# Performance work log

Measured on AMD Instinct MI355X. Metric: run time of the kernel, lower is better.

## Reference

```python
import jax, jax.numpy as jnp
import numpy as np

N_HEAD = 8


def _norm(x):
    # torch: (x - x.mean()) / x.std()  -- global, unbiased std (ddof=1)
    return (x - x.mean()) / x.std(ddof=1)


def _floyd_block2(x, w_qkv, scale):
    # x: [b, n, n, c]; w_qkv: [5c, c] (torch Linear weight layout)
    x = _norm(x)
    b, n, _, c = x.shape
    qkv = x @ w_qkv.T  # [b, n, n, 5c]
    q, k1, k2, v1, v2 = jnp.split(qkv, 5, axis=-1)

    def heads(t):  # 'b i j (h d) -> b h i j d'
        return t.reshape(b, n, n, N_HEAD, c // N_HEAD).transpose(0, 3, 1, 2, 4)

    q, k1, k2, v1, v2 = map(heads, (q, k1, k2, v1, v2))
    # pivotal attention: for pair (i,j) attend over pivot p with two k/v branches
    s = (jnp.einsum('bhijd,bhipd->bhijp', q, k1)
         + jnp.einsum('bhijd,bhpjd->bhijp', q, k2)) * scale  # [b,h,i,j,p]
    a = jax.nn.softmax(s, axis=-1)
    o = (jnp.einsum('bhijp,bhipd->bhijd', a, v1)
         + jnp.einsum('bhijp,bhpjd->bhijd', a, v2))
    # 'b h i j d -> b i j (h d)'
    return o.transpose(0, 2, 3, 1, 4).reshape(b, n, n, c)


def setup_inputs() -> dict:
    key = jax.random.key(0)
    k1, k2, k3, k4 = jax.random.split(key, 4)
    b, n, c, depth = 4, 96, 256, 4
    adj = jax.random.randint(k1, (b, n, n), 0, 2, dtype=jnp.int64)
    emb_w = jax.random.normal(k2, (128, c), dtype=jnp.float32)  # std 1.0 per init_weights
    qkv_w = jax.random.normal(k3, (depth, 5 * c, c), dtype=jnp.float32) * (c ** -0.5)
    head_w = jax.random.normal(k4, (c, c), dtype=jnp.float32) * 0.02
    head_b = jnp.zeros((c,), dtype=jnp.float32)
    return {'adj': adj, 'emb_w': emb_w, 'qkv_w': qkv_w,
            'head_w': head_w, 'head_b': head_b}


def reference(adj, emb_w, qkv_w, head_w, head_b):
    c = emb_w.shape[1]
    head_dim = c // N_HEAD
    scale = head_dim ** (-0.5) * 50.0  # FloydBlock2 scale
    x = emb_w[adj]  # [b, n, n, c]
    for l in range(qkv_w.shape[0]):
        x = _floyd_block2(x, qkv_w[l], scale)
    x = x.mean(axis=(1, 2))           # mean over (i, j) -> [b, c]
    x = jax.lax.stop_gradient(x)      # blocks run under torch.no_grad
    return x @ head_w.T + head_b
```

## Files before the change

### kernel.cpp

```cpp
#include <hip/hip_runtime.h>

#define B_ 4
#define N_ 96
#define C_ 256
#define NPAIR (B_*N_*N_)
#define CE (NPAIR*C_)
#define SCALE 8.838834764831844f
#define CP 132

typedef __attribute__((ext_vector_type(4))) float f32x4;
typedef __attribute__((ext_vector_type(8))) __bf16 bf16x8;
typedef __attribute__((ext_vector_type(4))) __bf16 bf16x4;
typedef __attribute__((ext_vector_type(4))) unsigned short u16x4;
typedef __attribute__((ext_vector_type(8))) unsigned short u16x8;

__device__ __forceinline__ unsigned short f2bf(float f){
  __bf16 h = (__bf16)f;
  return __builtin_bit_cast(unsigned short, h);
}
__device__ __forceinline__ float bf2f(unsigned short u){
  union { unsigned int i; float f; } v; v.i = ((unsigned int)u) << 16; return v.f;
}
__device__ __forceinline__ f32x4 vmax4(f32x4 a, f32x4 b){
  f32x4 r; r.x=fmaxf(a.x,b.x); r.y=fmaxf(a.y,b.y); r.z=fmaxf(a.z,b.z); r.w=fmaxf(a.w,b.w); return r;
}

__device__ __forceinline__ void gload16(const void* g, void* l){
  __builtin_amdgcn_global_load_lds((const __attribute__((address_space(1))) unsigned int*)g,
                                   (__attribute__((address_space(3))) unsigned int*)l,
                                   16, 0, 0);
}

__global__ __launch_bounds__(256) void k_init(float* __restrict__ z){
  for (int i = threadIdx.x; i < 1536; i += 256) z[i] = 0.f;
}

__global__ __launch_bounds__(256) void k_gather(const int* __restrict__ adj,
                                                const float* __restrict__ emb,
                                                unsigned short* __restrict__ xb,
                                                float2* __restrict__ part){
  int tid = threadIdx.x;
  int lp = tid >> 4, lane16 = tid & 15;
  int pair = blockIdx.x*16 + lp;
  int row = adj[pair];
  const f32x4* src = (const f32x4*)(emb + (size_t)row*C_);
  u16x4*       dst = (u16x4*)(xb + (size_t)pair*C_);
  float s = 0.f, q = 0.f;
  for (int v = 0; v < 4; ++v){
    f32x4 t = src[v*16 + lane16];
    u16x4 o;
    o.x = f2bf(t.x); o.y = f2bf(t.y); o.z = f2bf(t.z); o.w = f2bf(t.w);
    dst[v*16 + lane16] = o;
    s += t.x + t.y + t.z + t.w;
    q += t.x*t.x + t.y*t.y + t.z*t.z + t.w*t.w;
  }
  __shared__ float rs[256], rq[256];
  rs[tid] = s; rq[tid] = q; __syncthreads();
  for (int o = 128; o > 0; o >>= 1){
    if (tid < o){ rs[tid] += rs[tid+o]; rq[tid] += rq[tid+o]; }
    __syncthreads();
  }
  if (tid == 0){
    float* pp = (float*)&part[blockIdx.x & 63];
    atomicAdd(pp, rs[0]); atomicAdd(pp+1, rq[0]);
  }
}

__global__ __launch_bounds__(256) void k_wconv(const float* __restrict__ w,
                                               unsigned short* __restrict__ wb,
                                               float* __restrict__ wsum){
  int row  = blockIdx.x*4 + (threadIdx.x >> 6);
  int lane = threadIdx.x & 63;
  f32x4 v = ((const f32x4*)(w + (size_t)row*256))[lane];
  u16x4 o;
  o.x = f2bf(v.x); o.y = f2bf(v.y); o.z = f2bf(v.z); o.w = f2bf(v.w);
  ((u16x4*)(wb + (size_t)row*256))[lane] = o;
  float s = v.x + v.y + v.z + v.w;
  for (int m = 32; m > 0; m >>= 1) s += __shfl_down(s, m);
  if (lane == 0) wsum[row] = s;
}

__global__ __launch_bounds__(256) void k_gemm(const unsigned short* __restrict__ Xb,
                                              const unsigned short* __restrict__ W,
                                              const float* __restrict__ wsum_l,
                                              const float2* __restrict__ part,
                                              unsigned short* __restrict__ qkv5){
  __shared__ unsigned short smem[128*CP];
  unsigned short* As = smem;
  unsigned short* Bs = smem + 128*64;
  const int tid = threadIdx.x;
  const int w = tid >> 6, lane = tid & 63;
  const int quad = lane >> 4, l16 = lane & 15;
  const int L = blockIdx.x;
  const int xcd = L & 7, rest = L >> 3;
  const int nt = rest % 10, kt2 = rest / 10;
  const int m0 = (xcd + 8*kt2) * 128, n0 = nt * 128;
  const int mw = (w & 1) * 64, nw = (w >> 1) * 64;
  double S = 0.0, Q = 0.0;
  for (int i = 0; i < 64; ++i){ float2 pp = part[i]; S += (double)pp.x; Q += (double)pp.y; }
  const float mean = (float)(S / (double)CE);
  const float rstd = (float)(1.0 / sqrt((Q - S*S/(double)CE) / (double)(CE - 1)));
  f32x4 acc[4][4] = {};

  for (int kt = 0; kt < 256; kt += 64){
    const int rbase = w * 32;
    const int rowoff = lane >> 3;
    const int kg = (lane & 7) ^ rowoff;
    for (int i8 = 0; i8 < 4; ++i8){
      int row = rbase + i8*8 + rowoff;
      gload16(Xb + (size_t)(m0+row)*256 + kt + kg*8, &As[(rbase + i8*8)*64]);
      gload16(W  + (size_t)(n0+row)*256 + kt + kg*8, &Bs[(rbase + i8*8)*64]);
    }
    __syncthreads();
    for (int ks = 0; ks < 2; ++ks){
      bf16x8 af[4], bf[4];
      for (int t4 = 0; t4 < 4; ++t4){
        int rm = mw + t4*16 + l16;
        af[t4] = *(const bf16x8*)((const char*)As + rm*128 + ((((ks<<2)|quad) ^ (rm&7))*16));
        int rn = nw + t4*16 + l16;
        bf[t4] = *(const bf16x8*)((const char*)Bs + rn*128 + ((((ks<<2)|quad) ^ (rn&7))*16));
      }
      for (int mi = 0; mi < 4; ++mi)
        for (int ni = 0; ni < 4; ++ni)
          acc[mi][ni] = __builtin_amdgcn_mfma_f32_16x16x32_bf16(af[mi], bf[ni], acc[mi][ni], 0, 0, 0);
    }
    __syncthreads();
  }

  float ws[4];
  #pragma unroll
  for (int ni = 0; ni < 4; ++ni) ws[ni] = wsum_l[n0 + nw + ni*16 + l16];
  for (int mi = 0; mi < 4; ++mi)
    for (int ni = 0; ni < 4; ++ni)
      for (int r = 0; r < 4; ++r){
        int row = mw + mi*16 + quad*4 + r;
        int col = nw + ni*16 + l16;
        float val = rstd*(acc[mi][ni][r] - mean*ws[ni]);
        smem[row*CP + col] = f2bf(val);
      }
  __syncthreads();

  const int t_slab = n0 >> 8;
  const int hbase  = (n0 >> 5) & 7;
  unsigned short* slab = qkv5 + (size_t)t_slab*CE;
  const int trow = tid >> 4;
  const int tcol = (tid & 15) * 8;
  const int h  = hbase + (tcol >> 5);
  const int dd = tcol & 31;
  for (int pass = 0; pass < 8; ++pass){
    int row = pass*16 + trow;
    int gm = m0 + row;
    int b = gm / 9216; int rem = gm - b*9216;
    int ii = rem / 96, jj = rem - (rem/96)*96;
    u16x8 vv = *(const u16x8*)&smem[row*CP + tcol];
    *(u16x8*)&slab[(((size_t)(b*8+h)*96 + ii)*96 + jj)*32 + dd] = vv;
  }
}

__global__ __launch_bounds__(256) void k_scores1(const unsigned short* __restrict__ qkv5,
                                                 unsigned short* __restrict__ s1){
  __shared__ unsigned short Qs[96*40], Ks[96*40];
  __shared__ unsigned short Ss[96*100];
  int wg = blockIdx.x; int bh = wg/96, ic = wg - bh*96;
  int tid = threadIdx.x;
  size_t gslab = (size_t)wg*3072;
  const unsigned short* qp = qkv5 + 0*(size_t)CE + gslab;
  const unsigned short* kp = qkv5 + 1*(size_t)CE + gslab;
  for (int g = tid; g < 768; g += 256){
    int j = g >> 3, q4 = g & 7;
    *(u16x4*)&Qs[j*40 + q4*4] = *(const u16x4*)&qp[j*32 + q4*4];
    *(u16x4*)&Ks[j*40 + q4*4] = *(const u16x4*)&kp[j*32 + q4*4];
  }
  __syncthreads();
  int w = tid >> 6, lane = tid & 63, quad = lane >> 4, l16 = lane & 15;
  #pragma unroll
  for (int r = 0; r < 9; ++r){
    int tile = w*9 + r; int jt = tile/6, pt = tile - jt*6;
    bf16x8 a = *(const bf16x8*)((const char*)Qs + (jt*16 + l16)*80 + quad*16);
    bf16x8 b = *(const bf16x8*)((const char*)Ks + (pt*16 + l16)*80 + quad*16);
    f32x4 c = {0.f,0.f,0.f,0.f};
    c = __builtin_amdgcn_mfma_f32_16x16x32_bf16(a, b, c, 0, 0, 0);
    int col = pt*16 + l16;
    #pragma unroll
    for (int rr = 0; rr < 4; ++rr){
      int row = jt*16 + quad*4 + rr;
      _Float16 hv = (_Float16)(c[rr] * SCALE);
      Ss[row*100 + col] = __builtin_bit_cast(unsigned short, hv);
    }
  }
  __syncthreads();
  for (int g = tid; g < 1152; g += 256){
    int j = g / 12, c8 = g - j*12;
    *(u16x8*)&s1[((size_t)(bh*96 + j))*9216 + ic*96 + c8*8] = *(const u16x8*)&Ss[j*100 + c8*8];
  }
}

__global__ __launch_bounds__(256) void k_attn2(const unsigned short* __restrict__ qkv5,
                                               const unsigned short* __restrict__ s1,
                                               unsigned short* __restrict__ a_out,
                                               unsigned short* __restrict__ xb,
                                               float* __restrict__ poolAcc,
                                               int last){
  __shared__ unsigned short Qs[96*40];
  __shared__ unsigned short Ks[96*40];
  __shared__ unsigned short SsPb[96*104];
  __shared__ float Mx[192], Sx[192];
  __shared__ float poolL[32];
  unsigned short* Vd = Qs;
  int wg = blockIdx.x; int bh = wg/96, jj = wg - bh*96;
  int b = bh >> 3, h = bh & 7;
  int tid = threadIdx.x;
  int w = tid >> 6, lane = tid & 63, quad = lane >> 4, l16 = lane & 15;
  const unsigned short* qn  = qkv5 + 0*(size_t)CE;
  const unsigned short* k2n = qkv5 + 2*(size_t)CE;
  const unsigned short* v2n = qkv5 + 4*(size_t)CE;
  if (tid < 192){ Mx[tid] = -1e30f; Sx[tid] = 0.f; }
  if (tid < 32) poolL[tid] = 0.f;
  const unsigned short* s1g = s1 + ((size_t)bh*96 + jj)*9216;
  for (int k = w; k < 18; k += 4)
    gload16(s1g + k*512 + lane*8, &SsPb[k*512]);
  for (int g = tid; g < 768; g += 256){
    int r7 = g & 7, q4 = (g >> 3) & 7, a8 = g >> 6;
    int p = r7 + a8*8;
    size_t base = (((size_t)bh*96 + p)*96 + jj)*32 + q4*4;
    *(u16x4*)&Qs[p*40 + q4*4] = *(const u16x4*)&qn[base];
    *(u16x4*)&Ks[p*40 + q4*4] = *(const u16x4*)&k2n[base];
  }
  __syncthreads();
  f32x4 sc[9];
  #pragma unroll
  for (int r = 0; r < 9; ++r){
    int tile = w*9 + r; int it = tile/6, pt = tile - it*6;
    bf16x8 a = *(const bf16x8*)((const char*)Qs + (it*16 + l16)*80 + quad*16);
    bf16x8 bb = *(const bf16x8*)((const char*)Ks + (pt*16 + l16)*80 + quad*16);
    f32x4 c = {0.f,0.f,0.f,0.f};
    c = __builtin_amdgcn_mfma_f32_16x16x32_bf16(a, bb, c, 0, 0, 0);
    int col = pt*16 + l16;
    #pragma unroll
    for (int rr = 0; rr < 4; ++rr){
      int row = it*16 + quad*4 + rr;
      _Float16 hv = __builtin_bit_cast(_Float16, SsPb[row*96 + col]);
      sc[r][rr] = c[rr]*SCALE + (float)hv;
    }
  }
  const bool odd = (w & 1);
  const int itA = (w*9)/6, itB = itA + 1;
  const int slot = w & 1;
  f32x4 vA = {-1e30f,-1e30f,-1e30f,-1e30f}, vB = vA;
  #pragma unroll
  for (int r = 0; r < 9; ++r){
    bool inA = odd ? (r < 3) : (r < 6);
    if (inA) vA = vmax4(vA, sc[r]); else vB = vmax4(vB, sc[r]);
  }
  #pragma unroll
  for (int m = 1; m < 16; m <<= 1){
    f32x4 t;
    t.x=__shfl_xor(vA.x,m); t.y=__shfl_xor(vA.y,m); t.z=__shfl_xor(vA.z,m); t.w=__shfl_xor(vA.w,m);
    vA = vmax4(vA, t);
    t.x=__shfl_xor(vB.x,m); t.y=__shfl_xor(vB.y,m); t.z=__shfl_xor(vB.z,m); t.w=__shfl_xor(vB.w,m);
    vB = vmax4(vB, t);
  }
  if (l16 < 4){
    float va = (l16==0)?vA.x:(l16==1)?vA.y:(l16==2)?vA.z:vA.w;
    float vb = (l16==0)?vB.x:(l16==1)?vB.y:(l16==2)?vB.z:vB.w;
    Mx[(itA*16 + quad*4 + l16)*2 + slot] = va;
    Mx[(itB*16 + quad*4 + l16)*2 + slot] = vb;
  }
  __syncthreads();
  for (int g = tid; g < 768; g += 256){
    int r7 = g & 7, q4 = (g >> 3) & 7, a8 = g >> 6;
    int p = r7 + a8*8;
    u16x4 v = *(const u16x4*)&v2n[(((size_t)bh*96 + p)*96 + jj)*32 + q4*4];
    int d0 = q4*4;
    Vd[(d0+0)*100 + p] = v.x; Vd[(d0+1)*100 + p] = v.y;
    Vd[(d0+2)*100 + p] = v.z; Vd[(d0+3)*100 + p] = v.w;
  }
  f32x4 mA, mB;
  #pragma unroll
  for (int rr = 0; rr < 4; ++rr){
    float2 ta = *(const float2*)&Mx[(itA*16 + quad*4 + rr)*2];
    float2 tb = *(const float2*)&Mx[(itB*16 + quad*4 + rr)*2];
    mA[rr] = fmaxf(ta.x, ta.y); mB[rr] = fmaxf(tb.x, tb.y);
  }
  f32x4 sA = {0.f,0.f,0.f,0.f}, sB = {0.f,0.f,0.f,0.f};
  #pragma unroll
  for (int r = 0; r < 9; ++r){
    bool inA = odd ? (r < 3) : (r < 6);
    #pragma unroll
    for (int rr = 0; rr < 4; ++rr){
      float m = inA ? mA[rr] : mB[rr];
      float e = __expf(sc[r][rr] - m);
      sc[r][rr] = e;
      if (inA) sA[rr] += e; else sB[rr] += e;
    }
  }
  #pragma unroll
  for (int m = 1; m < 16; m <<= 1){
    f32x4 t;
    t.x=__shfl_xor(sA.x,m); t.y=__shfl_xor(sA.y,m); t.z=__shfl_xor(sA.z,m); t.w=__shfl_xor(sA.w,m);
    sA += t;
    t.x=__shfl_xor(sB.x,m); t.y=__shfl_xor(sB.y,m); t.z=__shfl_xor(sB.z,m); t.w=__shfl_xor(sB.w,m);
    sB += t;
  }
  if (l16 < 4){
    float va = (l16==0)?sA.x:(l16==1)?sA.y:(l16==2)?sA.z:sA.w;
    float vb = (l16==0)?sB.x:(l16==1)?sB.y:(l16==2)?sB.z:sB.w;
    Sx[(itA*16 + quad*4 + l16)*2 + slot] = va;
    Sx[(itB*16 + quad*4 + l16)*2 + slot] = vb;
  }
  __syncthreads();
  f32x4 iA, iB;
  #pragma unroll
  for (int rr = 0; rr < 4; ++rr){
    float2 ta = *(const float2*)&Sx[(itA*16 + quad*4 + rr)*2];
    float2 tb = *(const float2*)&Sx[(itB*16 + quad*4 + rr)*2];
    iA[rr] = 1.f/(ta.x + ta.y); iB[rr] = 1.f/(tb.x + tb.y);
  }
  #pragma unroll
  for (int r = 0; r < 9; ++r){
    int tile = w*9 + r; int it = tile/6, pt = tile - it*6;
    int col = pt*16 + l16;
    bool inA = odd ? (r < 3) : (r < 6);
    #pragma unroll
    for (int rr = 0; rr < 4; ++rr){
      int row = it*16 + quad*4 + rr;
      float inv = inA ? iA[rr] : iB[rr];
      SsPb[row*104 + col] = f2bf(sc[r][rr] * inv);
    }
  }
  __syncthreads();
  unsigned short* ap = a_out + (size_t)bh*96*9216 + (size_t)jj*96;
  for (int g = tid; g < 1152; g += 256){
    int i = g / 12, c = g - i*12;
    *(u16x8*)&ap[(size_t)i*9216 + c*8] = *(const u16x8*)&SsPb[i*104 + c*8];
  }
  #pragma unroll
  for (int r = 0; r < 3; ++r){
    int tile = w*3 + r; int it = tile >> 1, dt = tile & 1;
    f32x4 c = {0.f,0.f,0.f,0.f};
    #pragma unroll
    for (int kp3 = 0; kp3 < 3; ++kp3){
      bf16x8 a = *(const bf16x8*)((const char*)SsPb + (it*16 + l16)*208 + kp3*64 + quad*16);
      const char* vb = (const char*)Vd + (dt*16 + l16)*200 + kp3*64 + quad*16;
      bf16x4 lo = *(const bf16x4*)vb;
      bf16x4 hi = *(const bf16x4*)(vb + 8);
      bf16x8 bb = __builtin_shufflevector(lo, hi, 0,1,2,3,4,5,6,7);
      c = __builtin_amdgcn_mfma_f32_16x16x32_bf16(a, bb, c, 0, 0, 0);
    }
    int d = dt*16 + l16;
    if (!last){
      #pragma unroll
      for (int rr = 0; rr < 4; ++rr){
        int i = it*16 + quad*4 + rr;
        xb[(((size_t)b*96 + i)*96 + jj)*256 + h*32 + d] = f2bf(c[rr]);
      }
    } else {
      atomicAdd(&poolL[d], c[0] + c[1] + c[2] + c[3]);
    }
  }
  if (last){
    __syncthreads();
    if (tid < 32) atomicAdd(&poolAcc[b*256 + h*32 + tid], poolL[tid]);
  }
}

__global__ __launch_bounds__(256) void k_attn1(const unsigned short* __restrict__ a_in,
                                               const unsigned short* __restrict__ qkv5,
                                               unsigned short* __restrict__ xb,
                                               float2* __restrict__ statsPart,
                                               float* __restrict__ poolAcc,
                                               int last){
  __shared__ unsigned short As[96*104], Vd[32*100];
  __shared__ float redS[256], redQ[256];
  __shared__ float poolL[32];
  int wg = blockIdx.x; int bh = wg/96, ii = wg - bh*96;
  int b = bh >> 3, h = bh & 7;
  int tid = threadIdx.x;
  if (tid < 32) poolL[tid] = 0.f;
  const unsigned short* vp = qkv5 + 3*(size_t)CE + ((size_t)bh*96 + ii)*3072;
  for (int g = tid; g < 768; g += 256){
    int r7 = g & 7, q4 = (g >> 3) & 7, a8 = g >> 6;
    int p = r7 + a8*8;
    u16x4 v = *(const u16x4*)&vp[p*32 + q4*4];
    int d0 = q4*4;
    Vd[(d0+0)*100 + p] = v.x; Vd[(d0+1)*100 + p] = v.y;
    Vd[(d0+2)*100 + p] = v.z; Vd[(d0+3)*100 + p] = v.w;
  }
  const unsigned short* ain = a_in + ((size_t)bh*96 + ii)*9216;
  for (int g = tid; g < 1152; g += 256){
    int j = g / 12, c = g - j*12;
    *(u16x8*)&As[j*104 + c*8] = *(const u16x8*)&ain[j*96 + c*8];
  }
  __syncthreads();
  int w = tid >> 6, lane = tid & 63, quad = lane >> 4, l16 = lane & 15;
  float ls = 0.f, lq = 0.f;
  #pragma unroll
  for (int r = 0; r < 3; ++r){
    int tile = w*3 + r; int jt = tile >> 1, dt = tile & 1;
    f32x4 c = {0.f,0.f,0.f,0.f};
    #pragma unroll
    for (int kp3 = 0; kp3 < 3; ++kp3){
      bf16x8 a = *(const bf16x8*)((const char*)As + (jt*16 + l16)*208 + kp3*64 + quad*16);
      const char* vb = (const char*)Vd + (dt*16 + l16)*200 + kp3*64 + quad*16;
      bf16x4 lo = *(const bf16x4*)vb;
      bf16x4 hi = *(const bf16x4*)(vb + 8);
      bf16x8 bb = __builtin_shufflevector(lo, hi, 0,1,2,3,4,5,6,7);
      c = __builtin_amdgcn_mfma_f32_16x16x32_bf16(a, bb, c, 0, 0, 0);
    }
    int d = dt*16 + l16;
    if (!last){
      #pragma unroll
      for (int rr = 0; rr < 4; ++rr){
        int j = jt*16 + quad*4 + rr;
        size_t xi = (((size_t)b*96 + ii)*96 + j)*256 + h*32 + d;
        float val = bf2f(xb[xi]) + c[rr];
        xb[xi] = f2bf(val); ls += val; lq += val*val;
      }
    } else {
      atomicAdd(&poolL[d], c[0] + c[1] + c[2] + c[3]);
    }
  }
  if (!last){
    redS[tid] = ls; redQ[tid] = lq; __syncthreads();
    for (int o = 128; o > 0; o >>= 1){
      if (tid < o){ redS[tid] += redS[tid+o]; redQ[tid] += redQ[tid+o]; }
      __syncthreads();
    }
    if (tid == 0){
      float* pp = (float*)&statsPart[blockIdx.x & 63];
      atomicAdd(pp, redS[0]); atomicAdd(pp+1, redQ[0]);
    }
  } else {
    __syncthreads();
    if (tid < 32) atomicAdd(&poolAcc[b*256 + h*32 + tid], poolL[tid]);
  }
}

__global__ __launch_bounds__(256) void k_head(const float* __restrict__ poolAcc,
                                              const float* __restrict__ hw,
                                              const float* __restrict__ hb,
                                              float* __restrict__ out){
  int b = blockIdx.x, t = threadIdx.x;
  __shared__ float xm[256];
  xm[t] = poolAcc[b*256 + t] * (1.0f/9216.0f);
  __syncthreads();
  float o = hb[t];
  for (int c = 0; c < 256; ++c) o += xm[c] * hw[t*256 + c];
  out[b*256 + t] = o;
}

extern "C" void kernel_launch(void* const* d_in, const int* in_sizes, int n_in,
                              void* d_out, int out_size, void* d_ws, size_t ws_size,
                              hipStream_t stream){
  (void)in_sizes; (void)n_in; (void)out_size; (void)ws_size;
  const int*   adj  = (const int*)d_in[0];
  const float* emb  = (const float*)d_in[1];
  const float* qkvw = (const float*)d_in[2];
  const float* hw   = (const float*)d_in[3];
  const float* hb   = (const float*)d_in[4];

  char* p = (char*)d_ws;
  unsigned short* xb   = (unsigned short*)p; p += (size_t)CE*2;
  unsigned short* qkv5 = (unsigned short*)p; p += (size_t)5*CE*2;
  unsigned short* s1   = (unsigned short*)p; p += (size_t)32*96*9216*2;
  unsigned short* aP   = (unsigned short*)p; p += (size_t)32*96*9216*2;
  unsigned short* wbf  = (unsigned short*)p; p += (size_t)4*1280*256*2;
  float*          wsum = (float*)p;          p += (size_t)4*1280*4;
  float2*         part = (float2*)p;         p += 4*64*sizeof(float2);
  float*          pool = (float*)p;          p += 1024*sizeof(float);

  k_init  <<<dim3(1),     dim3(256), 0, stream>>>((float*)part);
  k_gather<<<dim3(2304),  dim3(256), 0, stream>>>(adj, emb, xb, part);
  k_wconv <<<dim3(1280),  dim3(256), 0, stream>>>(qkvw, wbf, wsum);
  for (int l = 0; l < 4; ++l){
    int last = (l == 3) ? 1 : 0;
    k_gemm   <<<dim3(2880),    dim3(256), 0, stream>>>(xb, wbf + (size_t)l*1280*256,
                                                       wsum + l*1280, part + l*64, qkv5);
    k_scores1<<<dim3(3072),    dim3(256), 0, stream>>>(qkv5, s1);
    k_attn2  <<<dim3(3072),    dim3(256), 0, stream>>>(qkv5, s1, aP, xb, pool, last);
    k_attn1  <<<dim3(3072),    dim3(256), 0, stream>>>(aP, qkv5, xb,
                                                       part + (l+1 < 4 ? (l+1)*64 : 0),
                                                       pool, last);
  }
  k_head<<<dim3(4), dim3(256), 0, stream>>>(pool, hw, hb, (float*)d_out);
}
```

Baseline: 646.2 us.

## Split each layer into two head-half chunks with ping-pong activation buffers

Each layer's GEMM and attention kernels now run in two chunks, each covering half the heads (alternating 128-column N tiles). Intermediates like qkv5, s1 and aP stay hot in L2/MALL between stages, and block-to-XCD mapping is remapped so blocks sharing a bh land on the same XCD. Activations ping-pong between two buffers so the second chunk's GEMM still reads the unmodified layer input. This doubles kernel launches and halves per-launch parallelism.

```diff
diff --git a/kernel.cpp b/kernel.cpp
--- a/kernel.cpp
+++ b/kernel.cpp
@@ -29,6 +29,12 @@
   __builtin_amdgcn_global_load_lds((const __attribute__((address_space(1))) unsigned int*)g,
                                    (__attribute__((address_space(3))) unsigned int*)l,
                                    16, 0, 0);
+}
+
+__device__ __forceinline__ void attn_decode(int L, int c, int& bh, int& sec){
+  int virt = (L & 7)*192 + (L >> 3);
+  int lbh = virt / 96; sec = virt - lbh*96;
+  bh = ((lbh >> 2) << 3) + 4*c + (lbh & 3);
 }
 
 __global__ __launch_bounds__(256) void k_init(float* __restrict__ z){
@@ -84,7 +90,8 @@
                                               const unsigned short* __restrict__ W,
                                               const float* __restrict__ wsum_l,
                                               const float2* __restrict__ part,
-                                              unsigned short* __restrict__ qkv5){
+                                              unsigned short* __restrict__ qkv5,
+                                              int c){
   __shared__ unsigned short smem[128*CP];
   unsigned short* As = smem;
   unsigned short* Bs = smem + 128*64;
@@ -93,7 +100,7 @@
   const int quad = lane >> 4, l16 = lane & 15;
   const int L = blockIdx.x;
   const int xcd = L & 7, rest = L >> 3;
-  const int nt = rest % 10, kt2 = rest / 10;
+  const int nt = (rest % 5)*2 + c, kt2 = rest / 5;
   const int m0 = (xcd + 8*kt2) * 128, n0 = nt * 128;
   const int mw = (w & 1) * 64, nw = (w >> 1) * 64;
   double S = 0.0, Q = 0.0;
@@ -158,12 +165,13 @@
 }
 
 __global__ __launch_bounds__(256) void k_scores1(const unsigned short* __restrict__ qkv5,
-                                                 unsigned short* __restrict__ s1){
+                                                 unsigned short* __restrict__ s1,
+                                                 int c){
   __shared__ unsigned short Qs[96*40], Ks[96*40];
   __shared__ unsigned short Ss[96*100];
-  int wg = blockIdx.x; int bh = wg/96, ic = wg - bh*96;
+  int bh, ic; attn_decode(blockIdx.x, c, bh, ic);
   int tid = threadIdx.x;
-  size_t gslab = (size_t)wg*3072;
+  size_t gslab = ((size_t)bh*96 + ic)*3072;
   const unsigned short* qp = qkv5 + 0*(size_t)CE + gslab;
   const unsigned short* kp = qkv5 + 1*(size_t)CE + gslab;
   for (int g = tid; g < 768; g += 256){
@@ -178,13 +186,13 @@
     int tile = w*9 + r; int jt = tile/6, pt = tile - jt*6;
     bf16x8 a = *(const bf16x8*)((const char*)Qs + (jt*16 + l16)*80 + quad*16);
     bf16x8 b = *(const bf16x8*)((const char*)Ks + (pt*16 + l16)*80 + quad*16);
-    f32x4 c = {0.f,0.f,0.f,0.f};
-    c = __builtin_amdgcn_mfma_f32_16x16x32_bf16(a, b, c, 0, 0, 0);
+    f32x4 cc = {0.f,0.f,0.f,0.f};
+    cc = __builtin_amdgcn_mfma_f32_16x16x32_bf16(a, b, cc, 0, 0, 0);
     int col = pt*16 + l16;
     #pragma unroll
     for (int rr = 0; rr < 4; ++rr){
       int row = jt*16 + quad*4 + rr;
-      _Float16 hv = (_Float16)(c[rr] * SCALE);
+      _Float16 hv = (_Float16)(cc[rr] * SCALE);
       Ss[row*100 + col] = __builtin_bit_cast(unsigned short, hv);
     }
   }
@@ -198,16 +206,16 @@
 __global__ __launch_bounds__(256) void k_attn2(const unsigned short* __restrict__ qkv5,
                                                const unsigned short* __restrict__ s1,
                                                unsigned short* __restrict__ a_out,
-                                               unsigned short* __restrict__ xb,
+                                               unsigned short* __restrict__ xout,
                                                float* __restrict__ poolAcc,
-                                               int last){
+                                               int last, int c){
   __shared__ unsigned short Qs[96*40];
   __shared__ unsigned short Ks[96*40];
   __shared__ unsigned short SsPb[96*104];
   __shared__ float Mx[192], Sx[192];
   __shared__ float poolL[32];
   unsigned short* Vd = Qs;
-  int wg = blockIdx.x; int bh = wg/96, jj = wg - bh*96;
+  int bh, jj; attn_decode(blockIdx.x, c, bh, jj);
   int b = bh >> 3, h = bh & 7;
   int tid = threadIdx.x;
   int w = tid >> 6, lane = tid & 63, quad = lane >> 4, l16 = lane & 15;
@@ -233,14 +241,14 @@
     int tile = w*9 + r; int it = tile/6, pt = tile - it*6;
     bf16x8 a = *(const bf16x8*)((const char*)Qs + (it*16 + l16)*80 + quad*16);
     bf16x8 bb = *(const bf16x8*)((const char*)Ks + (pt*16 + l16)*80 + quad*16);
-    f32x4 c = {0.f,0.f,0.f,0.f};
-    c = __builtin_amdgcn_mfma_f32_16x16x32_bf16(a, bb, c, 0, 0, 0);
+    f32x4 cc = {0.f,0.f,0.f,0.f};
+    cc = __builtin_amdgcn_mfma_f32_16x16x32_bf16(a, bb, cc, 0, 0, 0);
     int col = pt*16 + l16;
     #pragma unroll
     for (int rr = 0; rr < 4; ++rr){
       int row = it*16 + quad*4 + rr;
       _Float16 hv = __builtin_bit_cast(_Float16, SsPb[row*96 + col]);
-      sc[r][rr] = c[rr]*SCALE + (float)hv;
+      sc[r][rr] = cc[rr]*SCALE + (float)hv;
     }
   }
   const bool odd = (w & 1);
@@ -331,13 +339,13 @@
   __syncthreads();
   unsigned short* ap = a_out + (size_t)bh*96*9216 + (size_t)jj*96;
   for (int g = tid; g < 1152; g += 256){
-    int i = g / 12, c = g - i*12;
-    *(u16x8*)&ap[(size_t)i*9216 + c*8] = *(const u16x8*)&SsPb[i*104 + c*8];
+    int i = g / 12, cc = g - i*12;
+    *(u16x8*)&ap[(size_t)i*9216 + cc*8] = *(const u16x8*)&SsPb[i*104 + cc*8];
   }
   #pragma unroll
   for (int r = 0; r < 3; ++r){
     int tile = w*3 + r; int it = tile >> 1, dt = tile & 1;
-    f32x4 c = {0.f,0.f,0.f,0.f};
+    f32x4 cc = {0.f,0.f,0.f,0.f};
     #pragma unroll
     for (int kp3 = 0; kp3 < 3; ++kp3){
       bf16x8 a = *(const bf16x8*)((const char*)SsPb + (it*16 + l16)*208 + kp3*64 + quad*16);
@@ -345,17 +353,17 @@
       bf16x4 lo = *(const bf16x4*)vb;
       bf16x4 hi = *(const bf16x4*)(vb + 8);
       bf16x8 bb = __builtin_shufflevector(lo, hi, 0,1,2,3,4,5,6,7);
-      c = __builtin_amdgcn_mfma_f32_16x16x32_bf16(a, bb, c, 0, 0, 0);
+      cc = __builtin_amdgcn_mfma_f32_16x16x32_bf16(a, bb, cc, 0, 0, 0);
     }
     int d = dt*16 + l16;
     if (!last){
       #pragma unroll
       for (int rr = 0; rr < 4; ++rr){
         int i = it*16 + quad*4 + rr;
-        xb[(((size_t)b*96 + i)*96 + jj)*256 + h*32 + d] = f2bf(c[rr]);
+        xout[(((size_t)b*96 + i)*96 + jj)*256 + h*32 + d] = f2bf(cc[rr]);
       }
     } else {
-      atomicAdd(&poolL[d], c[0] + c[1] + c[2] + c[3]);
+      atomicAdd(&poolL[d], cc[0] + cc[1] + cc[2] + cc[3]);
     }
   }
   if (last){
@@ -366,14 +374,14 @@
 
 __global__ __launch_bounds__(256) void k_attn1(const unsigned short* __restrict__ a_in,
                                                const unsigned short* __restrict__ qkv5,
-                                               unsigned short* __restrict__ xb,
+                                               unsigned short* __restrict__ xout,
                                                float2* __restrict__ statsPart,
                                                float* __restrict__ poolAcc,
-                                               int last){
+                                               int last, int c){
   __shared__ unsigned short As[96*104], Vd[32*100];
   __shared__ float redS[256], redQ[256];
   __shared__ float poolL[32];
-  int wg = blockIdx.x; int bh = wg/96, ii = wg - bh*96;
+  int bh, ii; attn_decode(blockIdx.x, c, bh, ii);
   int b = bh >> 3, h = bh & 7;
   int tid = threadIdx.x;
   if (tid < 32) poolL[tid] = 0.f;
@@ -388,8 +396,8 @@
   }
   const unsigned short* ain = a_in + ((size_t)bh*96 + ii)*9216;
   for (int g = tid; g < 1152; g += 256){
-    int j = g / 12, c = g - j*12;
-    *(u16x8*)&As[j*104 + c*8] = *(const u16x8*)&ain[j*96 + c*8];
+    int j = g / 12, cc = g - j*12;
+    *(u16x8*)&As[j*104 + cc*8] = *(const u16x8*)&ain[j*96 + cc*8];
   }
   __syncthreads();
   int w = tid >> 6, lane = tid & 63, quad = lane >> 4, l16 = lane & 15;
@@ -397,7 +405,7 @@
   #pragma unroll
   for (int r = 0; r < 3; ++r){
     int tile = w*3 + r; int jt = tile >> 1, dt = tile & 1;
-    f32x4 c = {0.f,0.f,0.f,0.f};
+    f32x4 cc = {0.f,0.f,0.f,0.f};
     #pragma unroll
     for (int kp3 = 0; kp3 < 3; ++kp3){
       bf16x8 a = *(const bf16x8*)((const char*)As + (jt*16 + l16)*208 + kp3*64 + quad*16);
@@ -405,7 +413,7 @@
       bf16x4 lo = *(const bf16x4*)vb;
       bf16x4 hi = *(const bf16x4*)(vb + 8);
       bf16x8 bb = __builtin_shufflevector(lo, hi, 0,1,2,3,4,5,6,7);
-      c = __builtin_amdgcn_mfma_f32_16x16x32_bf16(a, bb, c, 0, 0, 0);
+      cc = __builtin_amdgcn_mfma_f32_16x16x32_bf16(a, bb, cc, 0, 0, 0);
     }
     int d = dt*16 + l16;
     if (!last){
@@ -413,11 +421,11 @@
       for (int rr = 0; rr < 4; ++rr){
         int j = jt*16 + quad*4 + rr;
         size_t xi = (((size_t)b*96 + ii)*96 + j)*256 + h*32 + d;
-        float val = bf2f(xb[xi]) + c[rr];
-        xb[xi] = f2bf(val); ls += val; lq += val*val;
+        float val = bf2f(xout[xi]) + cc[rr];
+        xout[xi] = f2bf(val); ls += val; lq += val*val;
       }
     } else {
-      atomicAdd(&poolL[d], c[0] + c[1] + c[2] + c[3]);
+      atomicAdd(&poolL[d], cc[0] + cc[1] + cc[2] + cc[3]);
     }
   }
   if (!last){
@@ -445,7 +453,7 @@
   xm[t] = poolAcc[b*256 + t] * (1.0f/9216.0f);
   __syncthreads();
   float o = hb[t];
-  for (int c = 0; c < 256; ++c) o += xm[c] * hw[t*256 + c];
+  for (int cc = 0; cc < 256; ++cc) o += xm[cc] * hw[t*256 + cc];
   out[b*256 + t] = o;
 }
 
@@ -460,7 +468,8 @@
   const float* hb   = (const float*)d_in[4];
 
   char* p = (char*)d_ws;
-  unsigned short* xb   = (unsigned short*)p; p += (size_t)CE*2;
+  unsigned short* xb0  = (unsigned short*)p; p += (size_t)CE*2;
+  unsigned short* xb1  = (unsigned short*)p; p += (size_t)CE*2;
   unsigned short* qkv5 = (unsigned short*)p; p += (size_t)5*CE*2;
   unsigned short* s1   = (unsigned short*)p; p += (size_t)32*96*9216*2;
   unsigned short* aP   = (unsigned short*)p; p += (size_t)32*96*9216*2;
@@ -470,17 +479,21 @@
   float*          pool = (float*)p;          p += 1024*sizeof(float);
 
   k_init  <<<dim3(1),     dim3(256), 0, stream>>>((float*)part);
-  k_gather<<<dim3(2304),  dim3(256), 0, stream>>>(adj, emb, xb, part);
+  k_gather<<<dim3(2304),  dim3(256), 0, stream>>>(adj, emb, xb0, part);
   k_wconv <<<dim3(1280),  dim3(256), 0, stream>>>(qkvw, wbf, wsum);
   for (int l = 0; l < 4; ++l){
     int last = (l == 3) ? 1 : 0;
-    k_gemm   <<<dim3(2880),    dim3(256), 0, stream>>>(xb, wbf + (size_t)l*1280*256,
-                                                       wsum + l*1280, part + l*64, qkv5);
-    k_scores1<<<dim3(3072),    dim3(256), 0, stream>>>(qkv5, s1);
-    k_attn2  <<<dim3(3072),    dim3(256), 0, stream>>>(qkv5, s1, aP, xb, pool, last);
-    k_attn1  <<<dim3(3072),    dim3(256), 0, stream>>>(aP, qkv5, xb,
-                                                       part + (l+1 < 4 ? (l+1)*64 : 0),
-                                                       pool, last);
+    unsigned short* xin  = (l & 1) ? xb1 : xb0;
+    unsigned short* xout = (l & 1) ? xb0 : xb1;
+    for (int c = 0; c < 2; ++c){
+      k_gemm   <<<dim3(1440), dim3(256), 0, stream>>>(xin, wbf + (size_t)l*1280*256,
+                                                      wsum + l*1280, part + l*64, qkv5, c);
+      k_scores1<<<dim3(1536), dim3(256), 0, stream>>>(qkv5, s1, c);
+      k_attn2  <<<dim3(1536), dim3(256), 0, stream>>>(qkv5, s1, aP, xout, pool, last, c);
+      k_attn1  <<<dim3(1536), dim3(256), 0, stream>>>(aP, qkv5, xout,
+                                                      part + (l+1 < 4 ? (l+1)*64 : 0),
+                                                      pool, last, c);
+    }
   }
   k_head<<<dim3(4), dim3(256), 0, stream>>>(pool, hw, hb, (float*)d_out);
 }
```

New measurement: 724.9 us. 12.2% more time.
